# Optimization experiments

Hardware: AMD Instinct MI355X
Metric: run time of the kernel (lower is better)

Reference implementation:

```python
import jax, jax.numpy as jnp
import numpy as np

EMBED_DIM = 4096
N_HEADS = 16
HEAD_DIM = 256
ROTARY_DIM = 64
SCALE_ATTN = 16.0  # sqrt(head_dim)
MASK_VAL = -65504.0


def setup_inputs() -> dict:
    key = jax.random.key(0)
    ks = jax.random.split(key, 5)
    B, S, D = 2, 2048, EMBED_DIM
    sc = 1.0 / np.sqrt(D)
    return {
        "hidden_states": jax.random.normal(ks[0], (B, S, D), dtype=jnp.float32),
        "Wq": jax.random.normal(ks[1], (D, D), dtype=jnp.float32) * sc,
        "Wk": jax.random.normal(ks[2], (D, D), dtype=jnp.float32) * sc,
        "Wv": jax.random.normal(ks[3], (D, D), dtype=jnp.float32) * sc,
        "Wo": jax.random.normal(ks[4], (D, D), dtype=jnp.float32) * sc,
        "position_ids": jnp.arange(S, dtype=jnp.int32),
    }


def _gptj_rope(x, position_ids):
    # x: [B, S, H, rotary_dim]; GPT-J interleaved (rotate_every_two) RoPE
    half = ROTARY_DIM // 2
    inv_freq = 1.0 / (10000.0 ** (jnp.arange(0, ROTARY_DIM, 2, dtype=jnp.float32) / ROTARY_DIM))
    sinusoid = position_ids.astype(jnp.float32)[:, None] * inv_freq[None, :]  # [S, half]
    sin = jnp.repeat(jnp.sin(sinusoid), 2, axis=-1)[None, :, None, :]  # [1,S,1,rot]
    cos = jnp.repeat(jnp.cos(sinusoid), 2, axis=-1)[None, :, None, :]
    x1 = x[..., 0::2]
    x2 = x[..., 1::2]
    rotated = jnp.stack([-x2, x1], axis=-1).reshape(x.shape)
    return x * cos + rotated * sin


def reference(hidden_states, Wq, Wk, Wv, Wo, position_ids):
    B, S, D = hidden_states.shape
    H, hd, rot = N_HEADS, HEAD_DIM, ROTARY_DIM

    q = (hidden_states @ Wq.T).reshape(B, S, H, hd)
    k = (hidden_states @ Wk.T).reshape(B, S, H, hd)
    v = (hidden_states @ Wv.T).reshape(B, S, H, hd)

    # rotary on first rotary_dim dims only
    q = jnp.concatenate([_gptj_rope(q[..., :rot], position_ids), q[..., rot:]], axis=-1)
    k = jnp.concatenate([_gptj_rope(k[..., :rot], position_ids), k[..., rot:]], axis=-1)

    q = q.transpose(0, 2, 1, 3)  # [B,H,S,hd]
    k = k.transpose(0, 2, 1, 3)
    v = v.transpose(0, 2, 1, 3)

    scores = jnp.einsum("bhqd,bhkd->bhqk", q, k)
    causal = jnp.tril(jnp.ones((S, S), dtype=bool))[None, None]
    # faithful to source: mask with -65504 BEFORE dividing by scale_attn
    scores = jnp.where(causal, scores, MASK_VAL) / SCALE_ATTN
    probs = jax.nn.softmax(scores, axis=-1)
    ctx = jnp.einsum("bhqk,bhkd->bhqd", probs, v)  # [B,H,S,hd]

    ctx = ctx.transpose(0, 2, 1, 3).reshape(B, S, D)
    return ctx @ Wo.T
```

## Files before the change

kernel.cpp:

```cpp
#include <hip/hip_runtime.h>
#include <stdint.h>

typedef unsigned short u16;
typedef short short8 __attribute__((ext_vector_type(8)));
typedef __bf16 bf16x8 __attribute__((ext_vector_type(8)));
typedef float f32x4 __attribute__((ext_vector_type(4)));

__device__ __forceinline__ u16 f2bf(float f) {
  uint32_t u = __float_as_uint(f);
  u += 0x7fffu + ((u >> 16) & 1u);
  return (u16)(u >> 16);
}
__device__ __forceinline__ float bf2f(u16 h) {
  return __uint_as_float(((uint32_t)h) << 16);
}
__device__ __forceinline__ f32x4 mfma16(short8 a, short8 b, f32x4 c) {
  return __builtin_amdgcn_mfma_f32_16x16x32_bf16(
      __builtin_bit_cast(bf16x8, a), __builtin_bit_cast(bf16x8, b), c, 0, 0, 0);
}
__device__ __forceinline__ uint32_t cvtpk_bf16(float lo, float hi) {
  uint32_t r;
  asm("v_cvt_pk_bf16_f32 %0, %1, %2" : "=v"(r) : "v"(lo), "v"(hi));
  return r;
}
__device__ __forceinline__ void gld_lds16(const u16* g, u16* lds_base) {
  __builtin_amdgcn_global_load_lds(
      (__attribute__((address_space(1))) void*)g,
      (__attribute__((address_space(3))) void*)lds_base, 16, 0, 0);
}
#define BAR() do { asm volatile("" ::: "memory"); \
                   __builtin_amdgcn_s_barrier(); \
                   asm volatile("" ::: "memory"); } while (0)

__global__ __launch_bounds__(256) void cvt_bf16(const float* __restrict__ s,
                                                u16* __restrict__ d) {
  int i = blockIdx.x * 256 + threadIdx.x;
  const float4* s4 = (const float4*)s;
  float4 a = s4[2 * i], b = s4[2 * i + 1];
  uint4 o;
  o.x = (uint32_t)f2bf(a.x) | ((uint32_t)f2bf(a.y) << 16);
  o.y = (uint32_t)f2bf(a.z) | ((uint32_t)f2bf(a.w) << 16);
  o.z = (uint32_t)f2bf(b.x) | ((uint32_t)f2bf(b.y) << 16);
  o.w = (uint32_t)f2bf(b.z) | ((uint32_t)f2bf(b.w) << 16);
  ((uint4*)d)[i] = o;
}

template <int MODE>
__global__ __launch_bounds__(512, 2) void gemm_nt(const u16* __restrict__ A,
                                                  const u16* __restrict__ W,
                                                  void* __restrict__ outp,
                                                  float oscale) {
  constexpr int Kd = 4096;
  __shared__ __align__(16) u16 As[2][2][8192];
  __shared__ __align__(16) u16 Bs[2][2][8192];
  const int tid = threadIdx.x;
  const int wid = tid >> 6, l = tid & 63;
  const int lg = (l >> 4) & 3, lc = l & 15;
  const int wm = wid >> 2, wn = wid & 3;
  const int bid0 = blockIdx.x;
  const int bid = (bid0 & 7) * 32 + (bid0 >> 3);
  const int m0 = (bid >> 4) * 256, n0 = (bid & 15) * 256;

  const int srow = tid >> 3;
  const int scol = ((tid & 7) ^ (srow & 7)) * 8;
  const int arow = m0 + srow;
  const int browb = n0 + ((srow >> 5) & 1) * 64 + (srow & 31);

#define STAGE_A(BUF, H, T) do { \
    const u16* g0 = A + (size_t)(arow + (H) * 64) * Kd + (T) * 64 + scol; \
    gld_lds16(g0, &As[BUF][H][wid * 512]); \
    gld_lds16(g0 + (size_t)128 * Kd, &As[BUF][H][4096 + wid * 512]); \
  } while (0)
#define STAGE_B(BUF, H, T) do { \
    const u16* g0 = W + (size_t)(browb + (H) * 32) * Kd + (T) * 64 + scol; \
    gld_lds16(g0, &Bs[BUF][H][wid * 512]); \
    gld_lds16(g0 + (size_t)128 * Kd, &Bs[BUF][H][4096 + wid * 512]); \
  } while (0)

  f32x4 acc[8][4];
#pragma unroll
  for (int i = 0; i < 8; ++i)
#pragma unroll
    for (int j = 0; j < 4; ++j) acc[i][j] = (f32x4)0.0f;

  const int axor = (lc & 7);

  short8 af[4][2], b0f[2][2], b1f[2][2];

#define LDA(MQ) do { \
    const char* Ab_ = (const char*)As[buf][MQ] + (wm * 64 + lc) * 128; \
    _Pragma("unroll") for (int f = 0; f < 4; ++f) \
      _Pragma("unroll") for (int kk = 0; kk < 2; ++kk) \
        af[f][kk] = *(const short8*)(Ab_ + f * 2048 + (((kk * 4 + lg) ^ axor) << 4)); \
  } while (0)
#define LDB(DST, NQ) do { \
    const char* Bb_ = (const char*)Bs[buf][NQ] + (wn * 32 + lc) * 128; \
    _Pragma("unroll") for (int g = 0; g < 2; ++g) \
      _Pragma("unroll") for (int kk = 0; kk < 2; ++kk) \
        DST[g][kk] = *(const short8*)(Bb_ + g * 2048 + (((kk * 4 + lg) ^ axor) << 4)); \
  } while (0)
#define MM(MQ, NQ, BF) do { \
    __builtin_amdgcn_s_setprio(1); \
    _Pragma("unroll") for (int f = 0; f < 4; ++f) \
      _Pragma("unroll") for (int g = 0; g < 2; ++g) \
        _Pragma("unroll") for (int kk = 0; kk < 2; ++kk) \
          acc[(MQ) * 4 + f][(NQ) * 2 + g] = \
              mfma16(af[f][kk], BF[g][kk], acc[(MQ) * 4 + f][(NQ) * 2 + g]); \
    __builtin_amdgcn_s_setprio(0); \
  } while (0)

  STAGE_A(0, 0, 0); STAGE_B(0, 1, 0); STAGE_B(0, 0, 0); STAGE_A(0, 1, 0);
  STAGE_A(1, 0, 1); STAGE_B(1, 1, 1);
  asm volatile("s_waitcnt vmcnt(4)" ::: "memory");
  BAR();

#pragma unroll 1
  for (int t = 0; t < 62; ++t) {
    const int buf = t & 1, nbuf = buf ^ 1;
    LDA(0); LDB(b0f, 0); STAGE_B(nbuf, 0, t + 1);
    BAR(); MM(0, 0, b0f); BAR();
    LDB(b1f, 1); STAGE_A(nbuf, 1, t + 1);
    BAR(); MM(0, 1, b1f); BAR();
    LDA(1); STAGE_A(buf, 0, t + 2);
    BAR(); MM(1, 1, b1f); BAR();
    STAGE_B(buf, 1, t + 2);
    asm volatile("s_waitcnt vmcnt(4)" ::: "memory");
    BAR(); MM(1, 0, b0f); BAR();
  }
  {
    const int buf = 0, nbuf = 1;
    LDA(0); LDB(b0f, 0); STAGE_B(nbuf, 0, 63);
    BAR(); MM(0, 0, b0f); BAR();
    LDB(b1f, 1); STAGE_A(nbuf, 1, 63);
    BAR(); MM(0, 1, b1f); BAR();
    LDA(1);
    BAR(); MM(1, 1, b1f); BAR();
    asm volatile("s_waitcnt vmcnt(0)" ::: "memory");
    BAR(); MM(1, 0, b0f); BAR();
  }
  {
    const int buf = 1;
    LDA(0); LDB(b0f, 0);
    BAR(); MM(0, 0, b0f); BAR();
    LDB(b1f, 1);
    BAR(); MM(0, 1, b1f); BAR();
    LDA(1);
    BAR(); MM(1, 1, b1f); BAR();
    BAR(); MM(1, 0, b0f); BAR();
  }
#undef MM
#undef LDB
#undef LDA
#undef STAGE_A
#undef STAGE_B

  const int gr0 = m0 + wm * 128, gc0 = n0 + wn * 64;
#pragma unroll
  for (int mf = 0; mf < 8; ++mf)
#pragma unroll
    for (int nf = 0; nf < 4; ++nf)
#pragma unroll
      for (int r = 0; r < 4; ++r) {
        float v = acc[mf][nf][r] * oscale;
        int gr = gr0 + mf * 16 + lg * 4 + r;
        int gc = gc0 + nf * 16 + lc;
        if constexpr (MODE == 0) {
          ((u16*)outp)[((size_t)(((gr >> 11) * 16 + (gc >> 8)) * 2048 +
                                 (gr & 2047))) * 256 + (gc & 255)] = f2bf(v);
        } else if constexpr (MODE == 1) {
          ((u16*)outp)[(size_t)((gr >> 11) * 4096 + gc) * 2048 + (gr & 2047)] =
              f2bf(v);
        } else {
          ((float*)outp)[(size_t)gr * 4096 + gc] = v;
        }
      }
}

__global__ __launch_bounds__(256) void rope_qk(u16* __restrict__ Qb,
                                               u16* __restrict__ Kb,
                                               const int* __restrict__ pos) {
  int idx = blockIdx.x * 256 + threadIdx.x;
  int pair = idx & 31;
  int s = (idx >> 5) & 2047;
  int bh = (idx >> 16) & 31;
  u16* T = (idx >> 21) ? Kb : Qb;
  float p = (float)pos[s];
  float inv = powf(10000.0f, -(float)pair * (1.0f / 32.0f));
  float ang = p * inv, sn, cs;
  sincosf(ang, &sn, &cs);
  u16* base = T + ((size_t)bh * 2048 + s) * 256 + pair * 2;
  float x1 = bf2f(base[0]), x2 = bf2f(base[1]);
  base[0] = f2bf(x1 * cs - x2 * sn);
  base[1] = f2bf(x2 * cs + x1 * sn);
}

__global__ __launch_bounds__(256) void flash_attn(const u16* __restrict__ Q,
                                                  const u16* __restrict__ K,
                                                  const u16* __restrict__ Vt,
                                                  u16* __restrict__ ctx) {
  __shared__ u16 Ks[2][32 * 256];
  __shared__ u16 Vs[2][256 * 32];
  __shared__ u16 P[4][16 * 40];

  const int bid = blockIdx.x;
  const int bidp = (bid & 7) * 128 + (bid >> 3);
  const int bh = bidp >> 5;
  const int qi = bidp & 31;
  const int q0 = 1984 - qi * 64;
  const int tid = threadIdx.x;
  const int wid = tid >> 6, l = tid & 63;
  const int lg = l >> 4, lc = l & 15;
  const int qr = q0 + wid * 16;

  const u16* Qh = Q + (size_t)bh * 2048 * 256;
  const u16* Kh = K + (size_t)bh * 2048 * 256;
  const u16* Vh = Vt + (size_t)bh * 256 * 2048;

  int krow[4], kcol[4], vrow[4], vcol[4];
#pragma unroll
  for (int jj = 0; jj < 4; ++jj) {
    int j = wid * 4 + jj;
    krow[jj] = 2 * j + (l >> 5);
    kcol[jj] = ((((l & 31) << 4) ^ ((krow[jj] & 7) << 4)) >> 1);
    vrow[jj] = j * 16 + (l >> 2);
    vcol[jj] = ((((l & 3) << 4) ^ (((vrow[jj] >> 1) & 3) << 4)) >> 1);
  }

  short8 qf[8];
#pragma unroll
  for (int kk = 0; kk < 8; ++kk)
    qf[kk] = *(const short8*)&Qh[(size_t)(qr + lc) * 256 + kk * 32 + lg * 8];

  f32x4 o[16];
#pragma unroll
  for (int nf = 0; nf < 16; ++nf) o[nf] = (f32x4)0.0f;
  float mrow = -1e30f;
  float lrow = 0.0f;

  uint32_t* Pw = (uint32_t*)P[wid];
  const u16* Pm = P[wid];

  const int ntiles = q0 / 32 + 2;

#pragma unroll
  for (int jj = 0; jj < 4; ++jj) {
    gld_lds16(Kh + (size_t)krow[jj] * 256 + kcol[jj], &Ks[0][(wid * 4 + jj) * 512]);
    gld_lds16(Vh + (size_t)vrow[jj] * 2048 + vcol[jj], &Vs[0][(wid * 4 + jj) * 512]);
  }
  __syncthreads();

  for (int t = 0; t < ntiles; ++t) {
    const int buf = t & 1;
    if (t + 1 < ntiles) {
      const int kv1 = (t + 1) << 5;
#pragma unroll
      for (int jj = 0; jj < 4; ++jj) {
        gld_lds16(Kh + (size_t)(kv1 + krow[jj]) * 256 + kcol[jj],
                  &Ks[buf ^ 1][(wid * 4 + jj) * 512]);
        gld_lds16(Vh + (size_t)vrow[jj] * 2048 + kv1 + vcol[jj],
                  &Vs[buf ^ 1][(wid * 4 + jj) * 512]);
      }
    }
    const int kv0 = t << 5;
    const char* KsB = (const char*)Ks[buf];
    const char* VsB = (const char*)Vs[buf];

    f32x4 s0 = (f32x4)0.0f, s1 = (f32x4)0.0f;
#pragma unroll
    for (int kk = 0; kk < 8; ++kk) {
      const int cb = kk * 64 + lg * 16;
      short8 k0 = *(const short8*)(KsB + lc * 512 + (cb ^ ((lc & 7) << 4)));
      short8 k1 = *(const short8*)(KsB + (16 + lc) * 512 + (cb ^ ((lc & 7) << 4)));
      s0 = mfma16(k0, qf[kk], s0);
      s1 = mfma16(k1, qf[kk], s1);
    }
    float sv[8];
#pragma unroll
    for (int r = 0; r < 4; ++r) { sv[r] = s0[r]; sv[4 + r] = s1[r]; }
    if (kv0 + 31 > qr) {
#pragma unroll
      for (int f = 0; f < 2; ++f)
#pragma unroll
        for (int r = 0; r < 4; ++r) {
          int kvg = kv0 + f * 16 + lg * 4 + r;
          if (kvg > qr + lc) sv[f * 4 + r] = -1e30f;
        }
    }
    float m8 = fmaxf(fmaxf(fmaxf(sv[0], sv[1]), fmaxf(sv[2], sv[3])),
                     fmaxf(fmaxf(sv[4], sv[5]), fmaxf(sv[6], sv[7])));
    float pm = fmaxf(m8, __shfl_xor(m8, 16));
    pm = fmaxf(pm, __shfl_xor(pm, 32));
    if (__ballot(pm > mrow)) {
      float mn = fmaxf(mrow, pm);
      float alpha = __builtin_amdgcn_exp2f(mrow - mn);
      lrow *= alpha;
      float aa[4];
#pragma unroll
      for (int r = 0; r < 4; ++r) aa[r] = __shfl(alpha, lg * 4 + r);
#pragma unroll
      for (int nf = 0; nf < 16; ++nf) {
        f32x4 t4 = o[nf];
#pragma unroll
        for (int r = 0; r < 4; ++r) t4[r] *= aa[r];
        o[nf] = t4;
      }
      mrow = mn;
    }
    float p[8];
#pragma unroll
    for (int j = 0; j < 8; ++j) p[j] = __builtin_amdgcn_exp2f(sv[j] - mrow);
    float ps = ((p[0] + p[1]) + (p[2] + p[3])) + ((p[4] + p[5]) + (p[6] + p[7]));
    ps += __shfl_xor(ps, 16);
    ps += __shfl_xor(ps, 32);
    lrow += ps;
    asm volatile("" ::: "memory");
    Pw[lc * 20 + lg * 2 + 0] = cvtpk_bf16(p[0], p[1]);
    Pw[lc * 20 + lg * 2 + 1] = cvtpk_bf16(p[2], p[3]);
    Pw[lc * 20 + 8 + lg * 2 + 0] = cvtpk_bf16(p[4], p[5]);
    Pw[lc * 20 + 8 + lg * 2 + 1] = cvtpk_bf16(p[6], p[7]);
    asm volatile("" ::: "memory");
    short8 pf = *(const short8*)&Pm[lc * 40 + lg * 8];
#pragma unroll
    for (int nf = 0; nf < 16; ++nf) {
      const int d = nf * 16 + lc;
      short8 vf = *(const short8*)(VsB + d * 64 + ((lg * 16) ^ (((d >> 1) & 3) << 4)));
      o[nf] = mfma16(pf, vf, o[nf]);
    }
    asm volatile("" ::: "memory");
    __syncthreads();
  }

  float il = 1.0f / lrow;
  float ia[4];
#pragma unroll
  for (int r = 0; r < 4; ++r) ia[r] = __shfl(il, lg * 4 + r);
  const int crow0 = (bh >> 4) * 2048 + qr;
  const int ccol0 = (bh & 15) * 256;
#pragma unroll
  for (int nf = 0; nf < 16; ++nf)
#pragma unroll
    for (int r = 0; r < 4; ++r)
      ctx[(size_t)(crow0 + lg * 4 + r) * 4096 + ccol0 + nf * 16 + lc] =
          f2bf(o[nf][r] * ia[r]);
}

extern "C" void kernel_launch(void* const* d_in, const int* in_sizes, int n_in,
                              void* d_out, int out_size, void* d_ws, size_t ws_size,
                              hipStream_t stream) {
  const float* hidden = (const float*)d_in[0];
  const float* Wq = (const float*)d_in[1];
  const float* Wk = (const float*)d_in[2];
  const float* Wv = (const float*)d_in[3];
  const float* Wo = (const float*)d_in[4];
  const int* pos = (const int*)d_in[5];

  const size_t NEL = 16777216;
  if (ws_size < 6 * NEL * sizeof(u16)) return;

  u16* hb = (u16*)d_ws;
  u16* wq = hb + NEL;
  u16* wk = wq + NEL;
  u16* wv = wk + NEL;
  u16* wo = wv + NEL;
  u16* vt = wo + NEL;
  u16* ctx = hb;
  u16* qb = (u16*)d_out;
  u16* kb = qb + NEL;

  cvt_bf16<<<8192, 256, 0, stream>>>(hidden, hb);
  cvt_bf16<<<8192, 256, 0, stream>>>(Wq, wq);
  cvt_bf16<<<8192, 256, 0, stream>>>(Wk, wk);
  cvt_bf16<<<8192, 256, 0, stream>>>(Wv, wv);
  cvt_bf16<<<8192, 256, 0, stream>>>(Wo, wo);

  gemm_nt<0><<<256, 512, 0, stream>>>(hb, wq, qb, 0.09016844f);
  gemm_nt<0><<<256, 512, 0, stream>>>(hb, wk, kb, 1.0f);
  gemm_nt<1><<<256, 512, 0, stream>>>(hb, wv, vt, 1.0f);

  rope_qk<<<16384, 256, 0, stream>>>(qb, kb, pos);

  flash_attn<<<1024, 256, 0, stream>>>(qb, kb, vt, ctx);

  gemm_nt<2><<<256, 512, 0, stream>>>(ctx, wo, d_out, 1.0f);
}
```

Before: 872.4 us.

## Process two 64-row query groups per attention block to reuse K/V tiles

Each flash-attention workgroup now handles 128 query rows as two 16-row sets per wave, sharing every loaded K/V LDS tile across both sets, and the grid is halved to 512 blocks. Block-to-(head, q-tile) mapping is reworked to pair long and short causal tiles per XCD for load balance. This cuts K/V global and LDS traffic per query. The cost is doubled accumulator and Q-fragment registers (oA/oB, qfA/qfB), which may lower occupancy or spill, and fewer blocks in flight.

```diff
diff --git a/kernel.cpp b/kernel.cpp
--- a/kernel.cpp
+++ b/kernel.cpp
@@ -202,15 +202,20 @@
   __shared__ u16 Vs[2][256 * 32];
   __shared__ u16 P[4][16 * 40];
 
-  const int bid = blockIdx.x;
-  const int bidp = (bid & 7) * 128 + (bid >> 3);
-  const int bh = bidp >> 5;
-  const int qi = bidp & 31;
-  const int q0 = 1984 - qi * 64;
+  const int bid0 = blockIdx.x;
+  const int xcd = bid0 & 7, j = bid0 >> 3;
+  const int r_ = j & 15;
+  const int top = j >> 5;
+  const int hl = top * 2 + ((j >> 4) & 1);
+  const int qi = top ? r_ : (15 - r_);
+  const int bh = xcd * 4 + hl;
+  const int q0 = qi * 128;
+
   const int tid = threadIdx.x;
   const int wid = tid >> 6, l = tid & 63;
   const int lg = l >> 4, lc = l & 15;
-  const int qr = q0 + wid * 16;
+  const int qrA = q0 + wid * 16;
+  const int qrB = q0 + 64 + wid * 16;
 
   const u16* Qh = Q + (size_t)bh * 2048 * 256;
   const u16* Kh = K + (size_t)bh * 2048 * 256;
@@ -219,28 +224,30 @@
   int krow[4], kcol[4], vrow[4], vcol[4];
 #pragma unroll
   for (int jj = 0; jj < 4; ++jj) {
-    int j = wid * 4 + jj;
-    krow[jj] = 2 * j + (l >> 5);
+    int c = wid * 4 + jj;
+    krow[jj] = 2 * c + (l >> 5);
     kcol[jj] = ((((l & 31) << 4) ^ ((krow[jj] & 7) << 4)) >> 1);
-    vrow[jj] = j * 16 + (l >> 2);
+    vrow[jj] = c * 16 + (l >> 2);
     vcol[jj] = ((((l & 3) << 4) ^ (((vrow[jj] >> 1) & 3) << 4)) >> 1);
   }
 
-  short8 qf[8];
-#pragma unroll
-  for (int kk = 0; kk < 8; ++kk)
-    qf[kk] = *(const short8*)&Qh[(size_t)(qr + lc) * 256 + kk * 32 + lg * 8];
-
-  f32x4 o[16];
-#pragma unroll
-  for (int nf = 0; nf < 16; ++nf) o[nf] = (f32x4)0.0f;
-  float mrow = -1e30f;
-  float lrow = 0.0f;
+  short8 qfA[8], qfB[8];
+#pragma unroll
+  for (int kk = 0; kk < 8; ++kk) {
+    qfA[kk] = *(const short8*)&Qh[(size_t)(qrA + lc) * 256 + kk * 32 + lg * 8];
+    qfB[kk] = *(const short8*)&Qh[(size_t)(qrB + lc) * 256 + kk * 32 + lg * 8];
+  }
+
+  f32x4 oA[16], oB[16];
+#pragma unroll
+  for (int nf = 0; nf < 16; ++nf) { oA[nf] = (f32x4)0.0f; oB[nf] = (f32x4)0.0f; }
+  float mrowA = -1e30f, lrowA = 0.0f;
+  float mrowB = -1e30f, lrowB = 0.0f;
 
   uint32_t* Pw = (uint32_t*)P[wid];
   const u16* Pm = P[wid];
 
-  const int ntiles = q0 / 32 + 2;
+  const int ntiles = q0 / 32 + 4;
 
 #pragma unroll
   for (int jj = 0; jj < 4; ++jj) {
@@ -265,83 +272,156 @@
     const char* KsB = (const char*)Ks[buf];
     const char* VsB = (const char*)Vs[buf];
 
-    f32x4 s0 = (f32x4)0.0f, s1 = (f32x4)0.0f;
+    f32x4 s0A = (f32x4)0.0f, s1A = (f32x4)0.0f;
+    f32x4 s0B = (f32x4)0.0f, s1B = (f32x4)0.0f;
 #pragma unroll
     for (int kk = 0; kk < 8; ++kk) {
       const int cb = kk * 64 + lg * 16;
       short8 k0 = *(const short8*)(KsB + lc * 512 + (cb ^ ((lc & 7) << 4)));
       short8 k1 = *(const short8*)(KsB + (16 + lc) * 512 + (cb ^ ((lc & 7) << 4)));
-      s0 = mfma16(k0, qf[kk], s0);
-      s1 = mfma16(k1, qf[kk], s1);
+      s0A = mfma16(k0, qfA[kk], s0A);
+      s1A = mfma16(k1, qfA[kk], s1A);
+      s0B = mfma16(k0, qfB[kk], s0B);
+      s1B = mfma16(k1, qfB[kk], s1B);
     }
-    float sv[8];
-#pragma unroll
-    for (int r = 0; r < 4; ++r) { sv[r] = s0[r]; sv[4 + r] = s1[r]; }
-    if (kv0 + 31 > qr) {
-#pragma unroll
-      for (int f = 0; f < 2; ++f)
-#pragma unroll
-        for (int r = 0; r < 4; ++r) {
-          int kvg = kv0 + f * 16 + lg * 4 + r;
-          if (kvg > qr + lc) sv[f * 4 + r] = -1e30f;
+
+    short8 pfA, pfB;
+    {
+      float sv[8];
+#pragma unroll
+      for (int r = 0; r < 4; ++r) { sv[r] = s0A[r]; sv[4 + r] = s1A[r]; }
+      if (kv0 + 31 > qrA) {
+#pragma unroll
+        for (int f = 0; f < 2; ++f)
+#pragma unroll
+          for (int r = 0; r < 4; ++r) {
+            int kvg = kv0 + f * 16 + lg * 4 + r;
+            if (kvg > qrA + lc) sv[f * 4 + r] = -1e30f;
+          }
+      }
+      float m8 = fmaxf(fmaxf(fmaxf(sv[0], sv[1]), fmaxf(sv[2], sv[3])),
+                       fmaxf(fmaxf(sv[4], sv[5]), fmaxf(sv[6], sv[7])));
+      float pm = fmaxf(m8, __shfl_xor(m8, 16));
+      pm = fmaxf(pm, __shfl_xor(pm, 32));
+      if (__ballot(pm > mrowA)) {
+        float mn = fmaxf(mrowA, pm);
+        float alpha = __builtin_amdgcn_exp2f(mrowA - mn);
+        lrowA *= alpha;
+        float aa[4];
+#pragma unroll
+        for (int r = 0; r < 4; ++r) aa[r] = __shfl(alpha, lg * 4 + r);
+#pragma unroll
+        for (int nf = 0; nf < 16; ++nf) {
+          f32x4 t4 = oA[nf];
+#pragma unroll
+          for (int r = 0; r < 4; ++r) t4[r] *= aa[r];
+          oA[nf] = t4;
         }
+        mrowA = mn;
+      }
+      float p[8];
+#pragma unroll
+      for (int q = 0; q < 8; ++q) p[q] = __builtin_amdgcn_exp2f(sv[q] - mrowA);
+      float ps = ((p[0] + p[1]) + (p[2] + p[3])) + ((p[4] + p[5]) + (p[6] + p[7]));
+      ps += __shfl_xor(ps, 16);
+      ps += __shfl_xor(ps, 32);
+      lrowA += ps;
+      asm volatile("" ::: "memory");
+      Pw[lc * 20 + lg * 2 + 0] = cvtpk_bf16(p[0], p[1]);
+      Pw[lc * 20 + lg * 2 + 1] = cvtpk_bf16(p[2], p[3]);
+      Pw[lc * 20 + 8 + lg * 2 + 0] = cvtpk_bf16(p[4], p[5]);
+      Pw[lc * 20 + 8 + lg * 2 + 1] = cvtpk_bf16(p[6], p[7]);
+      asm volatile("" ::: "memory");
+      pfA = *(const short8*)&Pm[lc * 40 + lg * 8];
+      asm volatile("" ::: "memory");
     }
-    float m8 = fmaxf(fmaxf(fmaxf(sv[0], sv[1]), fmaxf(sv[2], sv[3])),
-                     fmaxf(fmaxf(sv[4], sv[5]), fmaxf(sv[6], sv[7])));
-    float pm = fmaxf(m8, __shfl_xor(m8, 16));
-    pm = fmaxf(pm, __shfl_xor(pm, 32));
-    if (__ballot(pm > mrow)) {
-      float mn = fmaxf(mrow, pm);
-      float alpha = __builtin_amdgcn_exp2f(mrow - mn);
-      lrow *= alpha;
-      float aa[4];
-#pragma unroll
-      for (int r = 0; r < 4; ++r) aa[r] = __shfl(alpha, lg * 4 + r);
-#pragma unroll
-      for (int nf = 0; nf < 16; ++nf) {
-        f32x4 t4 = o[nf];
-#pragma unroll
-        for (int r = 0; r < 4; ++r) t4[r] *= aa[r];
-        o[nf] = t4;
-      }
-      mrow = mn;
+    {
+      float sv[8];
+#pragma unroll
+      for (int r = 0; r < 4; ++r) { sv[r] = s0B[r]; sv[4 + r] = s1B[r]; }
+      if (kv0 + 31 > qrB) {
+#pragma unroll
+        for (int f = 0; f < 2; ++f)
+#pragma unroll
+          for (int r = 0; r < 4; ++r) {
+            int kvg = kv0 + f * 16 + lg * 4 + r;
+            if (kvg > qrB + lc) sv[f * 4 + r] = -1e30f;
+          }
+      }
+      float m8 = fmaxf(fmaxf(fmaxf(sv[0], sv[1]), fmaxf(sv[2], sv[3])),
+                       fmaxf(fmaxf(sv[4], sv[5]), fmaxf(sv[6], sv[7])));
+      float pm = fmaxf(m8, __shfl_xor(m8, 16));
+      pm = fmaxf(pm, __shfl_xor(pm, 32));
+      if (__ballot(pm > mrowB)) {
+        float mn = fmaxf(mrowB, pm);
+        float alpha = __builtin_amdgcn_exp2f(mrowB - mn);
+        lrowB *= alpha;
+        float aa[4];
+#pragma unroll
+        for (int r = 0; r < 4; ++r) aa[r] = __shfl(alpha, lg * 4 + r);
+#pragma unroll
+        for (int nf = 0; nf < 16; ++nf) {
+          f32x4 t4 = oB[nf];
+#pragma unroll
+          for (int r = 0; r < 4; ++r) t4[r] *= aa[r];
+          oB[nf] = t4;
+        }
+        mrowB = mn;
+      }
+      float p[8];
+#pragma unroll
+      for (int q = 0; q < 8; ++q) p[q] = __builtin_amdgcn_exp2f(sv[q] - mrowB);
+      float ps = ((p[0] + p[1]) + (p[2] + p[3])) + ((p[4] + p[5]) + (p[6] + p[7]));
+      ps += __shfl_xor(ps, 16);
+      ps += __shfl_xor(ps, 32);
+      lrowB += ps;
+      asm volatile("" ::: "memory");
+      Pw[lc * 20 + lg * 2 + 0] = cvtpk_bf16(p[0], p[1]);
+      Pw[lc * 20 + lg * 2 + 1] = cvtpk_bf16(p[2], p[3]);
+      Pw[lc * 20 + 8 + lg * 2 + 0] = cvtpk_bf16(p[4], p[5]);
+      Pw[lc * 20 + 8 + lg * 2 + 1] = cvtpk_bf16(p[6], p[7]);
+      asm volatile("" ::: "memory");
+      pfB = *(const short8*)&Pm[lc * 40 + lg * 8];
+      asm volatile("" ::: "memory");
     }
-    float p[8];
-#pragma unroll
-    for (int j = 0; j < 8; ++j) p[j] = __builtin_amdgcn_exp2f(sv[j] - mrow);
-    float ps = ((p[0] + p[1]) + (p[2] + p[3])) + ((p[4] + p[5]) + (p[6] + p[7]));
-    ps += __shfl_xor(ps, 16);
-    ps += __shfl_xor(ps, 32);
-    lrow += ps;
-    asm volatile("" ::: "memory");
-    Pw[lc * 20 + lg * 2 + 0] = cvtpk_bf16(p[0], p[1]);
-    Pw[lc * 20 + lg * 2 + 1] = cvtpk_bf16(p[2], p[3]);
-    Pw[lc * 20 + 8 + lg * 2 + 0] = cvtpk_bf16(p[4], p[5]);
-    Pw[lc * 20 + 8 + lg * 2 + 1] = cvtpk_bf16(p[6], p[7]);
-    asm volatile("" ::: "memory");
-    short8 pf = *(const short8*)&Pm[lc * 40 + lg * 8];
 #pragma unroll
     for (int nf = 0; nf < 16; ++nf) {
       const int d = nf * 16 + lc;
       short8 vf = *(const short8*)(VsB + d * 64 + ((lg * 16) ^ (((d >> 1) & 3) << 4)));
-      o[nf] = mfma16(pf, vf, o[nf]);
+      oA[nf] = mfma16(pfA, vf, oA[nf]);
+      oB[nf] = mfma16(pfB, vf, oB[nf]);
     }
     asm volatile("" ::: "memory");
     __syncthreads();
   }
 
-  float il = 1.0f / lrow;
-  float ia[4];
-#pragma unroll
-  for (int r = 0; r < 4; ++r) ia[r] = __shfl(il, lg * 4 + r);
-  const int crow0 = (bh >> 4) * 2048 + qr;
   const int ccol0 = (bh & 15) * 256;
-#pragma unroll
-  for (int nf = 0; nf < 16; ++nf)
-#pragma unroll
-    for (int r = 0; r < 4; ++r)
-      ctx[(size_t)(crow0 + lg * 4 + r) * 4096 + ccol0 + nf * 16 + lc] =
-          f2bf(o[nf][r] * ia[r]);
+  {
+    float il = 1.0f / lrowA;
+    float ia[4];
+#pragma unroll
+    for (int r = 0; r < 4; ++r) ia[r] = __shfl(il, lg * 4 + r);
+    const int crow0 = (bh >> 4) * 2048 + qrA;
+#pragma unroll
+    for (int nf = 0; nf < 16; ++nf)
+#pragma unroll
+      for (int r = 0; r < 4; ++r)
+        ctx[(size_t)(crow0 + lg * 4 + r) * 4096 + ccol0 + nf * 16 + lc] =
+            f2bf(oA[nf][r] * ia[r]);
+  }
+  {
+    float il = 1.0f / lrowB;
+    float ia[4];
+#pragma unroll
+    for (int r = 0; r < 4; ++r) ia[r] = __shfl(il, lg * 4 + r);
+    const int crow0 = (bh >> 4) * 2048 + qrB;
+#pragma unroll
+    for (int nf = 0; nf < 16; ++nf)
+#pragma unroll
+      for (int r = 0; r < 4; ++r)
+        ctx[(size_t)(crow0 + lg * 4 + r) * 4096 + ccol0 + nf * 16 + lc] =
+            f2bf(oB[nf][r] * ia[r]);
+  }
 }
 
 extern "C" void kernel_launch(void* const* d_in, const int* in_sizes, int n_in,
@@ -379,7 +459,7 @@
 
   rope_qk<<<16384, 256, 0, stream>>>(qb, kb, pos);
 
-  flash_attn<<<1024, 256, 0, stream>>>(qb, kb, vt, ctx);
+  flash_attn<<<512, 256, 0, stream>>>(qb, kb, vt, ctx);
 
   gemm_nt<2><<<256, 512, 0, stream>>>(ctx, wo, d_out, 1.0f);
 }
```

New measurement: 946.9 us. +8.5%, slower.

## Merge GEMM main loop into two phases with fewer barriers

Applied to the files above, without the earlier changes.

Restructures the GEMM main loop from four barrier-separated MFMA phases to two, issuing both B fragment loads and two global stages per phase. This halves the barrier count per K-step, giving the scheduler larger MFMA blocks to interleave with memory ops. The cost is higher register pressure from holding both B fragments at once and coarser interleaving of loads with compute.

```diff
diff --git a/kernel.cpp b/kernel.cpp
--- a/kernel.cpp
+++ b/kernel.cpp
@@ -117,36 +117,29 @@
 #pragma unroll 1
   for (int t = 0; t < 62; ++t) {
     const int buf = t & 1, nbuf = buf ^ 1;
-    LDA(0); LDB(b0f, 0); STAGE_B(nbuf, 0, t + 1);
-    BAR(); MM(0, 0, b0f); BAR();
-    LDB(b1f, 1); STAGE_A(nbuf, 1, t + 1);
-    BAR(); MM(0, 1, b1f); BAR();
-    LDA(1); STAGE_A(buf, 0, t + 2);
-    BAR(); MM(1, 1, b1f); BAR();
-    STAGE_B(buf, 1, t + 2);
+    LDA(0); LDB(b0f, 0); LDB(b1f, 1);
+    STAGE_B(nbuf, 0, t + 1); STAGE_A(nbuf, 1, t + 1);
+    BAR(); MM(0, 0, b0f); MM(0, 1, b1f); BAR();
+    LDA(1);
+    STAGE_A(buf, 0, t + 2); STAGE_B(buf, 1, t + 2);
     asm volatile("s_waitcnt vmcnt(4)" ::: "memory");
-    BAR(); MM(1, 0, b0f); BAR();
+    BAR(); MM(1, 1, b1f); MM(1, 0, b0f); BAR();
   }
   {
     const int buf = 0, nbuf = 1;
-    LDA(0); LDB(b0f, 0); STAGE_B(nbuf, 0, 63);
-    BAR(); MM(0, 0, b0f); BAR();
-    LDB(b1f, 1); STAGE_A(nbuf, 1, 63);
-    BAR(); MM(0, 1, b1f); BAR();
+    LDA(0); LDB(b0f, 0); LDB(b1f, 1);
+    STAGE_B(nbuf, 0, 63); STAGE_A(nbuf, 1, 63);
+    BAR(); MM(0, 0, b0f); MM(0, 1, b1f); BAR();
     LDA(1);
-    BAR(); MM(1, 1, b1f); BAR();
     asm volatile("s_waitcnt vmcnt(0)" ::: "memory");
-    BAR(); MM(1, 0, b0f); BAR();
+    BAR(); MM(1, 1, b1f); MM(1, 0, b0f); BAR();
   }
   {
     const int buf = 1;
-    LDA(0); LDB(b0f, 0);
-    BAR(); MM(0, 0, b0f); BAR();
-    LDB(b1f, 1);
-    BAR(); MM(0, 1, b1f); BAR();
+    LDA(0); LDB(b0f, 0); LDB(b1f, 1);
+    BAR(); MM(0, 0, b0f); MM(0, 1, b1f); BAR();
     LDA(1);
-    BAR(); MM(1, 1, b1f); BAR();
-    BAR(); MM(1, 0, b0f); BAR();
+    BAR(); MM(1, 1, b1f); MM(1, 0, b0f); BAR();
   }
 #undef MM
 #undef LDB
```

Measured after the change: 747.4 us. -14.3%, faster.
